# Kernel optimization log

Hardware: AMD Instinct MI355X
Metric: run time of the kernel (lower is better)

## Reference

```python
import jax, jax.numpy as jnp
import numpy as np

TABLE_SIZE = 1_000_000
NUM_HASH = 4
EMB_DIM = 128
SEED = 42
SUB_DIM = EMB_DIM // NUM_HASH  # 32


def _hash_ids(ids, seed):
    """Vectorized integer hash (xxhash stand-in): 32-bit xorshift-multiply mix.
    ids: int32 array; seed: uint32 scalar. Returns int32 indices in [0, TABLE_SIZE).
    """
    x = ids.astype(jnp.uint32) + seed
    x = x ^ (x >> 16)
    x = x * jnp.uint32(0x7FEB352D)
    x = x ^ (x >> 15)
    x = x * jnp.uint32(0x846CA68B)
    x = x ^ (x >> 16)
    return (x % jnp.uint32(TABLE_SIZE)).astype(jnp.int32)


def setup_inputs() -> dict:
    key = jax.random.key(0)
    k_ids, k_tab = jax.random.split(key)
    input_ids = jax.random.randint(k_ids, (4096, 200), 0, 1_000_000_000, dtype=jnp.int32)
    # stacked per-hash embedding tables: [H, table_size, sub_dim]
    tables = jax.random.normal(k_tab, (NUM_HASH, TABLE_SIZE, SUB_DIM), dtype=jnp.float32)
    return {"input_ids": input_ids, "tables": tables}


def reference(input_ids, tables):
    orig_shape = input_ids.shape
    flat_ids = input_ids.reshape(-1)                       # [N]
    seeds = jnp.uint32(SEED) + jnp.arange(NUM_HASH, dtype=jnp.uint32)  # [H]
    # hashed indices per table: [H, N]
    idx = jax.vmap(lambda s: _hash_ids(flat_ids, s))(seeds)
    # per-table gather: [H, N, sub_dim]
    emb = jax.vmap(lambda tab, i: tab[i])(tables, idx)
    # concat along feature dim -> [N, H*sub_dim] == [N, EMB_DIM]
    out = jnp.moveaxis(emb, 0, 1).reshape(flat_ids.shape[0], EMB_DIM)
    return out.reshape(orig_shape + (EMB_DIM,))
```

## Files before the change

kernel.cpp:

```cpp
#include <hip/hip_runtime.h>
#include <cstdint>


#define TABLE_SIZE 1000000u
#define SEED 42u

typedef float vfloat4 __attribute__((ext_vector_type(4)));

__device__ __forceinline__ uint32_t hash_id(uint32_t x) {
    x ^= x >> 16;
    x *= 0x7FEB352Du;
    x ^= x >> 15;
    x *= 0x846CA68Bu;
    x ^= x >> 16;
    return x % TABLE_SIZE;
}

__global__ void __launch_bounds__(256) warm_kernel(const vfloat4* __restrict__ tab,
                                                   int nvec) {
    float acc = 0.0f;
    const int stride = gridDim.x * blockDim.x;
    for (int i = blockIdx.x * blockDim.x + threadIdx.x; i < nvec; i += stride) {
        const vfloat4 v = tab[i];
        acc += v.x + v.y + v.z + v.w;
    }
    asm volatile("" :: "v"(acc));
}

__global__ void __launch_bounds__(256) gather_kernel(const int* __restrict__ ids,
                                                     const vfloat4* __restrict__ tab,
                                                     vfloat4* __restrict__ out,
                                                     int n, uint32_t seed_h, int h) {
    const int tid = blockIdx.x * blockDim.x + threadIdx.x;
    const int gid = tid >> 3;
    if (gid >= n) return;
    const int d4 = tid & 7;

    const uint32_t idx = hash_id((uint32_t)ids[gid] + seed_h);
    const vfloat4 v = tab[(size_t)idx * 8 + (size_t)d4];
    __builtin_nontemporal_store(v, &out[(size_t)gid * 32 + (size_t)(h * 8 + d4)]);
}

extern "C" void kernel_launch(void* const* d_in, const int* in_sizes, int n_in,
                              void* d_out, int out_size, void* d_ws, size_t ws_size,
                              hipStream_t stream) {
    const int*     ids    = (const int*)d_in[0];
    const vfloat4* tables = (const vfloat4*)d_in[1];
    vfloat4*       out    = (vfloat4*)d_out;

    const int n = in_sizes[0];
    const int nvec = (int)(TABLE_SIZE * 8u);

    const long long gthreads = (long long)n * 8;
    const int gblock = 256;
    const int ggrid  = (int)((gthreads + gblock - 1) / gblock);

    for (int h = 0; h < 4; ++h) {
        const vfloat4* tab = tables + (size_t)h * TABLE_SIZE * 8;
        warm_kernel<<<2048, 256, 0, stream>>>(tab, nvec);
        gather_kernel<<<ggrid, gblock, 0, stream>>>(ids, tab, out, n,
                                                    SEED + (uint32_t)h, h);
    }
}
```

Baseline: 826.0 us.

## Bucket-sort hashed lookups by table row before gathering embeddings

Replaces the per-table warm-then-gather loop with a counting sort of all (table row, output slot) records into 8192 row buckets: histogram, single-block scan, atomic scatter, then one gather in bucket order. The goal is to give the random table reads locality so rows within a bucket share L2/MALL lines, and to drop the full-table warm pass. The cost is extra passes over the ids and a write and read of an 8-byte record per lookup, heavy atomics on the bucket cursors, and output writes that become scattered. A fused single-kernel gather is kept as a fallback when the workspace is too small.

```diff
diff --git a/kernel.cpp b/kernel.cpp
--- a/kernel.cpp
+++ b/kernel.cpp
@@ -4,6 +4,8 @@
 
 #define TABLE_SIZE 1000000u
 #define SEED 42u
+#define NB 8192
+#define BSHIFT 9
 
 typedef float vfloat4 __attribute__((ext_vector_type(4)));
 
@@ -16,29 +18,93 @@
     return x % TABLE_SIZE;
 }
 
-__global__ void __launch_bounds__(256) warm_kernel(const vfloat4* __restrict__ tab,
-                                                   int nvec) {
-    float acc = 0.0f;
-    const int stride = gridDim.x * blockDim.x;
-    for (int i = blockIdx.x * blockDim.x + threadIdx.x; i < nvec; i += stride) {
-        const vfloat4 v = tab[i];
-        acc += v.x + v.y + v.z + v.w;
-    }
-    asm volatile("" :: "v"(acc));
+__global__ void __launch_bounds__(256) zero_kernel(unsigned int* __restrict__ p, int n) {
+    int i = blockIdx.x * blockDim.x + threadIdx.x;
+    if (i < n) p[i] = 0u;
 }
 
-__global__ void __launch_bounds__(256) gather_kernel(const int* __restrict__ ids,
-                                                     const vfloat4* __restrict__ tab,
-                                                     vfloat4* __restrict__ out,
-                                                     int n, uint32_t seed_h, int h) {
+__global__ void __launch_bounds__(256) hist_kernel(const int* __restrict__ ids,
+                                                   unsigned int* __restrict__ hist,
+                                                   int n) {
+    int i = blockIdx.x * blockDim.x + threadIdx.x;
+    const int stride = gridDim.x * blockDim.x;
+    for (; i < n; i += stride) {
+        const uint32_t id = (uint32_t)ids[i];
+        #pragma unroll
+        for (uint32_t h = 0; h < 4; ++h) {
+            const uint32_t key = h * TABLE_SIZE + hash_id(id + SEED + h);
+            atomicAdd(&hist[key >> BSHIFT], 1u);
+        }
+    }
+}
+
+__global__ void __launch_bounds__(1024) scan_kernel(const unsigned int* __restrict__ hist,
+                                                    unsigned int* __restrict__ cursor) {
+    __shared__ unsigned int lds[1024];
+    const int t = threadIdx.x;
+    unsigned int v[8];
+    unsigned int s = 0;
+    #pragma unroll
+    for (int k = 0; k < 8; ++k) { v[k] = hist[t * 8 + k]; s += v[k]; }
+    lds[t] = s;
+    __syncthreads();
+    for (int off = 1; off < 1024; off <<= 1) {
+        unsigned int x = (t >= off) ? lds[t - off] : 0u;
+        __syncthreads();
+        lds[t] += x;
+        __syncthreads();
+    }
+    unsigned int base = (t == 0) ? 0u : lds[t - 1];
+    #pragma unroll
+    for (int k = 0; k < 8; ++k) { cursor[t * 8 + k] = base; base += v[k]; }
+}
+
+__global__ void __launch_bounds__(256) scatter_kernel(const int* __restrict__ ids,
+                                                      unsigned int* __restrict__ cursor,
+                                                      uint2* __restrict__ recs,
+                                                      int n) {
+    int i = blockIdx.x * blockDim.x + threadIdx.x;
+    const int stride = gridDim.x * blockDim.x;
+    for (; i < n; i += stride) {
+        const uint32_t id = (uint32_t)ids[i];
+        #pragma unroll
+        for (uint32_t h = 0; h < 4; ++h) {
+            const uint32_t key = h * TABLE_SIZE + hash_id(id + SEED + h);
+            const unsigned int pos = atomicAdd(&cursor[key >> BSHIFT], 1u);
+            recs[pos] = make_uint2(key, ((uint32_t)i << 2) | h);
+        }
+    }
+}
+
+__global__ void __launch_bounds__(256) sorted_gather_kernel(
+        const uint2* __restrict__ recs,
+        const vfloat4* __restrict__ tab,
+        vfloat4* __restrict__ out,
+        int R) {
     const int tid = blockIdx.x * blockDim.x + threadIdx.x;
-    const int gid = tid >> 3;
-    if (gid >= n) return;
+    const int r = tid >> 3;
+    if (r >= R) return;
     const int d4 = tid & 7;
 
-    const uint32_t idx = hash_id((uint32_t)ids[gid] + seed_h);
-    const vfloat4 v = tab[(size_t)idx * 8 + (size_t)d4];
-    __builtin_nontemporal_store(v, &out[(size_t)gid * 32 + (size_t)(h * 8 + d4)]);
+    const uint2 rec = recs[r];
+    const vfloat4 v = tab[(size_t)rec.x * 8 + (size_t)d4];
+    __builtin_nontemporal_store(
+        v, &out[(size_t)(rec.y >> 2) * 32 + (size_t)((rec.y & 3u) * 8u + d4)]);
+}
+
+__global__ void __launch_bounds__(256) bloom_emb_kernel(const int* __restrict__ ids,
+                                                        const vfloat4* __restrict__ tables,
+                                                        vfloat4* __restrict__ out,
+                                                        int n) {
+    const int tid = blockIdx.x * blockDim.x + threadIdx.x;
+    const int gid = tid >> 5;
+    if (gid >= n) return;
+    const int lane = tid & 31;
+    const int h  = lane >> 3;
+    const int d4 = lane & 7;
+    const uint32_t idx = hash_id((uint32_t)ids[gid] + SEED + (uint32_t)h);
+    const vfloat4 v = tables[((size_t)h * TABLE_SIZE + idx) * 8 + (size_t)d4];
+    out[(size_t)gid * 32 + (size_t)lane] = v;
 }
 
 extern "C" void kernel_launch(void* const* d_in, const int* in_sizes, int n_in,
@@ -49,16 +115,28 @@
     vfloat4*       out    = (vfloat4*)d_out;
 
     const int n = in_sizes[0];
-    const int nvec = (int)(TABLE_SIZE * 8u);
+    const int R = n * 4;
 
-    const long long gthreads = (long long)n * 8;
-    const int gblock = 256;
-    const int ggrid  = (int)((gthreads + gblock - 1) / gblock);
+    const size_t recs_bytes = (size_t)R * 8;
+    const size_t need = recs_bytes + 2 * NB * sizeof(unsigned int) + 256;
 
-    for (int h = 0; h < 4; ++h) {
-        const vfloat4* tab = tables + (size_t)h * TABLE_SIZE * 8;
-        warm_kernel<<<2048, 256, 0, stream>>>(tab, nvec);
-        gather_kernel<<<ggrid, gblock, 0, stream>>>(ids, tab, out, n,
-                                                    SEED + (uint32_t)h, h);
+    if (ws_size < need) {
+        const long long total = (long long)n * 32;
+        const int grid = (int)((total + 255) / 256);
+        bloom_emb_kernel<<<grid, 256, 0, stream>>>(ids, tables, out, n);
+        return;
     }
+
+    uint2*        recs   = (uint2*)d_ws;
+    unsigned int* hist   = (unsigned int*)((char*)d_ws + ((recs_bytes + 255) & ~(size_t)255));
+    unsigned int* cursor = hist + NB;
+
+    zero_kernel<<<(NB + 255) / 256, 256, 0, stream>>>(hist, NB);
+    hist_kernel<<<2048, 256, 0, stream>>>(ids, hist, n);
+    scan_kernel<<<1, 1024, 0, stream>>>(hist, cursor);
+    scatter_kernel<<<2048, 256, 0, stream>>>(ids, cursor, recs, n);
+
+    const long long gthreads = (long long)R * 8;
+    const int ggrid = (int)((gthreads + 255) / 256);
+    sorted_gather_kernel<<<ggrid, 256, 0, stream>>>(recs, tables, out, R);
 }
```

After: 1.050 ms. 1.27x slower.
